# Kernel optimization log

Measured on AMD Instinct MI355X. Metric: run time of the kernel, lower is better.

Reference implementation:

```python
import jax, jax.numpy as jnp
import numpy as np

HIDDEN = 2048
HEAD_DIM = 128
N_HEADS = 16
ROPE_THETA = 150000.0
EPS = 1e-5
SEQ = 2048


def setup_inputs() -> dict:
    key = jax.random.key(0)
    k0, k1, k2 = jax.random.split(key, 3)
    x = jax.random.normal(k0, (SEQ, HIDDEN), jnp.float32)
    norm_scale = jnp.ones((HIDDEN,), jnp.float32)
    qkv_w = jax.random.normal(k1, (3 * HIDDEN, HIDDEN), jnp.float32) * 0.02
    qkv_b = jnp.zeros((3 * HIDDEN,), jnp.float32)
    out_w = jax.random.normal(k2, (HIDDEN, HIDDEN), jnp.float32) * 0.02
    out_b = jnp.zeros((HIDDEN,), jnp.float32)
    return {"x": x, "norm_scale": norm_scale, "qkv_w": qkv_w, "qkv_b": qkv_b,
            "out_w": out_w, "out_b": out_b}


def _rmsnorm(x, scale, eps=EPS):
    t = x * jax.lax.rsqrt(jnp.mean(x * x, axis=-1, keepdims=True) + eps)
    return t * scale


def _apply_rotary(x, cos, sin):
    # x: (n, H, d); cos/sin: (n, 1, d//2)  -- NeoX half-split rotary
    x1, x2 = jnp.split(x, 2, axis=-1)
    return jnp.concatenate([x1 * cos - x2 * sin, x2 * cos + x1 * sin], axis=-1)


def reference(x, norm_scale, qkv_w, qkv_b, out_w, out_b):
    n = x.shape[0]
    t = _rmsnorm(x, norm_scale)
    qkv = t @ qkv_w.T + qkv_b                      # (n, 3*hidden)
    q, k, v = jnp.split(qkv, 3, axis=-1)           # each (n, hidden)
    q = q.reshape(n, N_HEADS, HEAD_DIM)
    k = k.reshape(n, N_HEADS, HEAD_DIM)
    v = v.reshape(n, N_HEADS, HEAD_DIM)

    pos = jnp.arange(n, dtype=jnp.float32)
    inv = 1.0 / (ROPE_THETA ** (jnp.arange(0, HEAD_DIM, 2, dtype=jnp.float32) / HEAD_DIM))
    freqs = pos[:, None] * inv[None, :]            # (n, d//2)
    cos = jnp.cos(freqs)[:, None, :]
    sin = jnp.sin(freqs)[:, None, :]
    q = _apply_rotary(q, cos, sin)
    k = _apply_rotary(k, cos, sin)

    scale = 1.0 / np.sqrt(HEAD_DIM)
    att = jnp.einsum('qhd,khd->hqk', q, k) * scale  # (H, n, n) -- full score tensor as in source
    causal = jnp.tril(jnp.ones((n, n), dtype=bool))
    att = jnp.where(causal[None, :, :], att, -jnp.inf)
    w = jax.nn.softmax(att, axis=-1)
    o = jnp.einsum('hqk,khd->qhd', w, v).reshape(n, HIDDEN)
    return x + o @ out_w.T + out_b
```

## Files before the change

### kernel.cpp

```cpp
#include <hip/hip_runtime.h>
#include <math.h>

#define HIDDEN 2048
#define NHEADS 16
#define HD     128
#define QKV3   6144
#define EPSV   1e-5f
#define NEGBIG -30000.0f

typedef short bf16x8 __attribute__((ext_vector_type(8)));
typedef float f32x4  __attribute__((ext_vector_type(4)));

__device__ inline unsigned short f2bf(float f) {
    unsigned u = __float_as_uint(f);
    u += 0x7fff + ((u >> 16) & 1);
    return (unsigned short)(u >> 16);
}
__device__ inline float bf2f(unsigned short h) {
    return __uint_as_float(((unsigned)h) << 16);
}

union FragCast { uint4 u; bf16x8 v; };
__device__ inline bf16x8 as_frag(uint4 x) { FragCast c; c.u = x; return c.v; }
union U16x8 { unsigned short h[8]; uint4 v; };

__device__ __forceinline__ void gload16(const void* gsrc, void* ldst) {
    typedef __attribute__((address_space(1))) const char GC;
    typedef __attribute__((address_space(3))) char LC;
    __builtin_amdgcn_global_load_lds((GC*)(unsigned long long)gsrc,
                                     (LC*)(unsigned long long)ldst, 16, 0, 0);
}

__global__ __launch_bounds__(256) void f32_to_bf16_kernel(
        const float* __restrict__ in, unsigned short* __restrict__ out, int count) {
    int i = (blockIdx.x * 256 + threadIdx.x) * 4;
    if (i >= count) return;
    float4 v = *(const float4*)&in[i];
    ushort4 o = {f2bf(v.x), f2bf(v.y), f2bf(v.z), f2bf(v.w)};
    *(ushort4*)&out[i] = o;
}

__global__ void rope_table_kernel(float* __restrict__ cost, float* __restrict__ sint) {
    int pos = blockIdx.x;
    int i   = threadIdx.x;
    float inv = exp2f((float)i * (-17.1946030f / 64.0f));
    float f   = (float)pos * inv;
    cost[pos * 64 + i] = cosf(f);
    sint[pos * 64 + i] = sinf(f);
}

__global__ __launch_bounds__(256) void rmsnorm_kernel(
        const float* __restrict__ x, const float* __restrict__ scale,
        unsigned short* __restrict__ t) {
    int row = blockIdx.x;
    int tid = threadIdx.x;
    const float* xr = x + (size_t)row * HIDDEN;
    unsigned short* tr = t + (size_t)row * HIDDEN;

    float4 v[2];
    float ss = 0.f;
#pragma unroll
    for (int u = 0; u < 2; ++u) {
        v[u] = ((const float4*)xr)[tid + u * 256];
        ss += v[u].x * v[u].x + v[u].y * v[u].y + v[u].z * v[u].z + v[u].w * v[u].w;
    }
#pragma unroll
    for (int off = 32; off; off >>= 1) ss += __shfl_xor(ss, off);
    __shared__ float wsum[4];
    if ((tid & 63) == 0) wsum[tid >> 6] = ss;
    __syncthreads();
    float tot = wsum[0] + wsum[1] + wsum[2] + wsum[3];
    float r = rsqrtf(tot / (float)HIDDEN + EPSV);
#pragma unroll
    for (int u = 0; u < 2; ++u) {
        int idx = tid + u * 256;
        float4 sc = ((const float4*)scale)[idx];
        ushort4 o = {f2bf(v[u].x * r * sc.x), f2bf(v[u].y * r * sc.y),
                     f2bf(v[u].z * r * sc.z), f2bf(v[u].w * r * sc.w)};
        ((ushort4*)tr)[idx] = o;
    }
}

__global__ __launch_bounds__(256) void gemm_bf16_kernel(
        const unsigned short* __restrict__ A, const unsigned short* __restrict__ B,
        const float* __restrict__ bias, const float* __restrict__ resid,
        float* __restrict__ C, int M, int N, int K) {
    __shared__ __align__(16) unsigned short As[128][32];
    __shared__ __align__(16) unsigned short Bs[128][32];

    int tid  = threadIdx.x;
    int bn   = blockIdx.x * 128;
    int bm   = blockIdx.y * 128;
    int lane = tid & 63;
    int wid  = tid >> 6;
    int wr   = wid >> 1;
    int wc   = wid & 1;
    int fr   = lane & 15;
    int fq   = lane >> 4;

    f32x4 acc[4][4] = {};

    const int nk = K >> 5;
    for (int kt = 0; kt < nk; ++kt) {
        int k0 = kt << 5;
#pragma unroll
        for (int u = 0; u < 2; ++u) {
            int c   = tid + u * 256;
            int row = c >> 2;
            int kk  = (c & 3) * 8;
            gload16(&A[(size_t)(bm + row) * K + k0 + kk], &As[(wid << 4) + (u << 6)][0]);
            gload16(&B[(size_t)(bn + row) * K + k0 + kk], &Bs[(wid << 4) + (u << 6)][0]);
        }
        __syncthreads();

        bf16x8 af[4], bfr[4];
#pragma unroll
        for (int i = 0; i < 4; ++i) {
            af[i]  = as_frag(*(const uint4*)&As[wr * 64 + i * 16 + fr][fq * 8]);
            bfr[i] = as_frag(*(const uint4*)&Bs[wc * 64 + i * 16 + fr][fq * 8]);
        }
#pragma unroll
        for (int mi = 0; mi < 4; ++mi)
#pragma unroll
            for (int ni = 0; ni < 4; ++ni)
                acc[mi][ni] = __builtin_amdgcn_mfma_f32_16x16x32_bf16(
                    af[mi], bfr[ni], acc[mi][ni], 0, 0, 0);
        __syncthreads();
    }

#pragma unroll
    for (int ni = 0; ni < 4; ++ni) {
        int col = bn + wc * 64 + ni * 16 + fr;
        float bb = bias[col];
#pragma unroll
        for (int mi = 0; mi < 4; ++mi) {
#pragma unroll
            for (int r = 0; r < 4; ++r) {
                int row = bm + wr * 64 + mi * 16 + fq * 4 + r;
                float v = acc[mi][ni][r] + bb;
                if (resid) v += resid[(size_t)row * N + col];
                C[(size_t)row * N + col] = v;
            }
        }
    }
}

__global__ void repack_qk_kernel(const float* __restrict__ qkv,
                                 const float* __restrict__ cost,
                                 const float* __restrict__ sint,
                                 unsigned short* __restrict__ qb,
                                 unsigned short* __restrict__ kb, int n) {
    int pos = blockIdx.x, h = blockIdx.y;
    int t = threadIdx.x;
    int qk = t >> 6, i = t & 63;
    const float* src = qkv + (size_t)pos * QKV3 + qk * HIDDEN + h * HD;
    float c = cost[pos * 64 + i], s = sint[pos * 64 + i];
    float x1 = src[i], x2 = src[i + 64];
    float y1 = x1 * c - x2 * s, y2 = x2 * c + x1 * s;
    float sc = qk ? 1.0f : 0.088388347648318447f;
    unsigned short* dst = (qk ? kb : qb) + ((size_t)h * n + pos) * HD;
    dst[i]      = f2bf(y1 * sc);
    dst[i + 64] = f2bf(y2 * sc);
}

__global__ __launch_bounds__(256) void v_transpose_kernel(
        const float* __restrict__ qkv, unsigned short* __restrict__ vt, int n) {
    int n0 = blockIdx.x * 64;
    int d0 = blockIdx.y * 64;
    int h  = blockIdx.z;
    __shared__ float tile[64][68];
    int tid = threadIdx.x;
#pragma unroll
    for (int u = 0; u < 4; ++u) {
        int c = tid + u * 256;
        int r = c >> 4, c4 = (c & 15) * 4;
        *(float4*)&tile[r][c4] =
            *(const float4*)&qkv[(size_t)(n0 + r) * QKV3 + 2 * HIDDEN + h * HD + d0 + c4];
    }
    __syncthreads();
#pragma unroll
    for (int u = 0; u < 2; ++u) {
        int c = tid + u * 256;
        int d = c >> 3, nn = (c & 7) * 8;
        U16x8 o;
#pragma unroll
        for (int e = 0; e < 8; ++e) o.h[e] = f2bf(tile[nn + e][d]);
        *(uint4*)&vt[((size_t)h * HD + d0 + d) * n + n0 + nn] = o.v;
    }
}

#define QB  128
#define KVB 64
#define NSPLIT 4
__global__ __launch_bounds__(512) void attn_part_kernel(
        const unsigned short* __restrict__ qb_,
        const unsigned short* __restrict__ kb,
        const unsigned short* __restrict__ vt,
        unsigned short* __restrict__ o_part,
        float* __restrict__ m_part,
        float* __restrict__ l_part, int n) {
    int nqb  = n / QB;
    int fid  = blockIdx.x;
    int h    = fid & 15;
    int rest = fid >> 4;
    int qbi  = (nqb - 1) - (rest % nqb);
    int s    = rest / nqb;
    int q0   = qbi * QB;
    int ntiles = (q0 + QB) / KVB;
    int chunk  = (ntiles + NSPLIT - 1) >> 2;
    int t0 = s * chunk;
    int t1 = t0 + chunk; if (t1 > ntiles) t1 = ntiles;
    int tid = threadIdx.x;

    if (t0 >= ntiles) {
        if (tid < QB) {
            size_t idx = ((size_t)s * NHEADS + h) * n + q0 + tid;
            m_part[idx] = NEGBIG;
            l_part[idx] = 0.f;
            for (int e = 0; e < HD / 8; ++e) {
                U16x8 z; z.v = make_uint4(0, 0, 0, 0);
                *(uint4*)&o_part[idx * HD + e * 8] = z.v;
            }
        }
        return;
    }

    int lane = tid & 63, w = tid >> 6;
    int g = lane >> 4, i = lane & 15;
    int myrow0 = q0 + w * 16;

    __shared__ __align__(16) unsigned short Kb[KVB][136];
    __shared__ __align__(16) unsigned short Vt[128][72];
    __shared__ __align__(16) unsigned short Pl[8][16][72];

    bf16x8 qf[4];
    {
        const unsigned short* qrow = qb_ + ((size_t)h * n + myrow0 + i) * HD;
#pragma unroll
        for (int kk = 0; kk < 4; ++kk)
            qf[kk] = as_frag(*(const uint4*)&qrow[kk * 32 + 8 * g]);
    }

    f32x4 o_acc[8] = {};
    float m_r[4], l_r[4];
#pragma unroll
    for (int r = 0; r < 4; ++r) { m_r[r] = 0.f; l_r[r] = 0.f; }

    for (int kt = t0; kt < t1; ++kt) {
        int k0 = kt * KVB;
#pragma unroll
        for (int u = 0; u < 2; ++u) {
            int c = tid + u * 512;
            int row = c >> 4, col = (c & 15) * 8;
            *(uint4*)&Kb[row][col] =
                *(const uint4*)&kb[((size_t)h * n + k0 + row) * HD + col];
        }
#pragma unroll
        for (int u = 0; u < 2; ++u) {
            int c = tid + u * 512;
            int row = c >> 3, col = (c & 7) * 8;
            *(uint4*)&Vt[row][col] =
                *(const uint4*)&vt[((size_t)h * HD + row) * n + k0 + col];
        }
        __syncthreads();

        f32x4 s_acc[4] = {};
#pragma unroll
        for (int nb = 0; nb < 4; ++nb)
#pragma unroll
            for (int kk = 0; kk < 4; ++kk) {
                bf16x8 kf = as_frag(*(const uint4*)&Kb[nb * 16 + i][kk * 32 + 8 * g]);
                s_acc[nb] = __builtin_amdgcn_mfma_f32_16x16x32_bf16(
                    qf[kk], kf, s_acc[nb], 0, 0, 0);
            }

        bool diagzone = (kt >= ntiles - 2);
        float mx[4];
#pragma unroll
        for (int r = 0; r < 4; ++r) mx[r] = NEGBIG;
#pragma unroll
        for (int nb = 0; nb < 4; ++nb)
#pragma unroll
            for (int r = 0; r < 4; ++r) {
                float sv = s_acc[nb][r];
                if (diagzone && (k0 + nb * 16 + i > myrow0 + 4 * g + r)) sv = NEGBIG;
                s_acc[nb][r] = sv;
                mx[r] = fmaxf(mx[r], sv);
            }
#pragma unroll
        for (int off = 1; off < 16; off <<= 1)
#pragma unroll
            for (int r = 0; r < 4; ++r)
                mx[r] = fmaxf(mx[r], __shfl_xor(mx[r], off));

        float alpha[4], sum[4];
#pragma unroll
        for (int r = 0; r < 4; ++r) {
            float mnew = fmaxf(m_r[r], mx[r]);
            alpha[r] = __expf(m_r[r] - mnew);
            m_r[r] = mnew;
            sum[r] = 0.f;
        }
#pragma unroll
        for (int nb = 0; nb < 4; ++nb)
#pragma unroll
            for (int r = 0; r < 4; ++r) {
                float p = __expf(s_acc[nb][r] - m_r[r]);
                s_acc[nb][r] = p;
                sum[r] += p;
            }
#pragma unroll
        for (int off = 1; off < 16; off <<= 1)
#pragma unroll
            for (int r = 0; r < 4; ++r)
                sum[r] += __shfl_xor(sum[r], off);
#pragma unroll
        for (int r = 0; r < 4; ++r) l_r[r] = l_r[r] * alpha[r] + sum[r];

#pragma unroll
        for (int d0 = 0; d0 < 8; ++d0)
#pragma unroll
            for (int r = 0; r < 4; ++r)
                o_acc[d0][r] *= alpha[r];

#pragma unroll
        for (int nb = 0; nb < 4; ++nb)
#pragma unroll
            for (int r = 0; r < 4; ++r)
                Pl[w][4 * g + r][nb * 16 + i] = f2bf(s_acc[nb][r]);
        __builtin_amdgcn_sched_barrier(0);

#pragma unroll
        for (int kk = 0; kk < 2; ++kk) {
            bf16x8 pf = as_frag(*(const uint4*)&Pl[w][i][kk * 32 + 8 * g]);
#pragma unroll
            for (int d0 = 0; d0 < 8; ++d0) {
                bf16x8 vf = as_frag(*(const uint4*)&Vt[d0 * 16 + i][kk * 32 + 8 * g]);
                o_acc[d0] = __builtin_amdgcn_mfma_f32_16x16x32_bf16(
                    pf, vf, o_acc[d0], 0, 0, 0);
            }
        }
        __syncthreads();
    }

#pragma unroll
    for (int r = 0; r < 4; ++r) {
        int q = myrow0 + 4 * g + r;
        size_t idx = ((size_t)s * NHEADS + h) * n + q;
#pragma unroll
        for (int d0 = 0; d0 < 8; ++d0)
            o_part[idx * HD + d0 * 16 + i] = f2bf(o_acc[d0][r]);
        if (i == 0) { m_part[idx] = m_r[r]; l_part[idx] = l_r[r]; }
    }
}

__global__ __launch_bounds__(256) void attn_combine_kernel(
        const unsigned short* __restrict__ o_part,
        const float* __restrict__ m_part, const float* __restrict__ l_part,
        unsigned short* __restrict__ ob, int n) {
    int q = blockIdx.x;
    int t = threadIdx.x;
    int h = t >> 4;
    int d = (t & 15) * 8;

    float m[NSPLIT], mstar = NEGBIG;
#pragma unroll
    for (int s = 0; s < NSPLIT; ++s) {
        m[s] = m_part[((size_t)s * NHEADS + h) * n + q];
        mstar = fmaxf(mstar, m[s]);
    }
    float l = 0.f, o[8] = {};
#pragma unroll
    for (int s = 0; s < NSPLIT; ++s) {
        if (m[s] < -1e4f) continue;
        float ws = __expf(m[s] - mstar);
        l += ws * l_part[((size_t)s * NHEADS + h) * n + q];
        U16x8 ov;
        ov.v = *(const uint4*)&o_part[(((size_t)s * NHEADS + h) * n + q) * HD + d];
#pragma unroll
        for (int e = 0; e < 8; ++e) o[e] += ws * bf2f(ov.h[e]);
    }
    float inv = 1.f / l;
    U16x8 w8;
#pragma unroll
    for (int e = 0; e < 8; ++e) w8.h[e] = f2bf(o[e] * inv);
    *(uint4*)&ob[(size_t)q * HIDDEN + h * HD + d] = w8.v;
}

extern "C" void kernel_launch(void* const* d_in, const int* in_sizes, int n_in,
                              void* d_out, int out_size, void* d_ws, size_t ws_size,
                              hipStream_t stream) {
    const float* x     = (const float*)d_in[0];
    const float* nsc   = (const float*)d_in[1];
    const float* qkv_w = (const float*)d_in[2];
    const float* qkv_b = (const float*)d_in[3];
    const float* out_w = (const float*)d_in[4];
    const float* out_b = (const float*)d_in[5];
    float* out = (float*)d_out;
    int n = in_sizes[0] / HIDDEN;

    char* w = (char*)d_ws;
    float* qkv  = (float*)w;  w += (size_t)n * QKV3 * 4;
    float* cost = (float*)w;  w += (size_t)n * 64 * 4;
    float* sint = (float*)w;  w += (size_t)n * 64 * 4;
    unsigned short* wq = (unsigned short*)w;
    unsigned short* qb = wq;
    unsigned short* kb = qb + (size_t)n * HIDDEN;
    unsigned short* vt = kb + (size_t)n * HIDDEN;
    size_t unionBytes = (size_t)QKV3 * HIDDEN * 2;
    size_t need3      = (size_t)3 * n * HIDDEN * 2;
    w += (unionBytes > need3 ? unionBytes : need3);
    unsigned short* wo = (unsigned short*)w;  w += (size_t)HIDDEN * HIDDEN * 2;
    unsigned short* tb = (unsigned short*)w;
    unsigned short* ob = tb;

    unsigned short* o_part = (unsigned short*)qkv;
    float* m_part = (float*)((char*)qkv + (size_t)NSPLIT * NHEADS * n * HD * 2);
    float* l_part = m_part + (size_t)NSPLIT * NHEADS * n;

    f32_to_bf16_kernel<<<(QKV3 * HIDDEN) / 1024, 256, 0, stream>>>(qkv_w, wq, QKV3 * HIDDEN);
    f32_to_bf16_kernel<<<(HIDDEN * HIDDEN) / 1024, 256, 0, stream>>>(out_w, wo, HIDDEN * HIDDEN);
    rope_table_kernel<<<n, 64, 0, stream>>>(cost, sint);
    rmsnorm_kernel<<<n, 256, 0, stream>>>(x, nsc, tb);
    gemm_bf16_kernel<<<dim3(QKV3 / 128, n / 128), 256, 0, stream>>>(
        tb, wq, qkv_b, nullptr, qkv, n, QKV3, HIDDEN);
    repack_qk_kernel<<<dim3(n, NHEADS), 128, 0, stream>>>(qkv, cost, sint, qb, kb, n);
    v_transpose_kernel<<<dim3(n / 64, HD / 64, NHEADS), 256, 0, stream>>>(qkv, vt, n);
    attn_part_kernel<<<dim3((n / QB) * NHEADS * NSPLIT), 512, 0, stream>>>(
        qb, kb, vt, o_part, m_part, l_part, n);
    attn_combine_kernel<<<n, 256, 0, stream>>>(o_part, m_part, l_part, ob, n);
    gemm_bf16_kernel<<<dim3(HIDDEN / 128, n / 128), 256, 0, stream>>>(
        ob, wo, out_b, x, out, n, HIDDEN, HIDDEN);
}
```

Before: 270.3 us.

## Double-buffer GEMM LDS tiles with async prefetch two stages ahead

Converts the bf16 GEMM's single shared-memory tile into a two-slot ring. Global-to-LDS loads for tile kt+2 are issued while MFMAs run on the current tile, with explicit vmcnt waits and barriers replacing __syncthreads. The goal is to hide global load latency behind compute. It doubles LDS use per block, which may lower occupancy, and it relies on hand-counted vmcnt values being correct for gload16.

```diff
diff --git a/kernel.cpp b/kernel.cpp
--- a/kernel.cpp
+++ b/kernel.cpp
@@ -85,8 +85,8 @@
         const unsigned short* __restrict__ A, const unsigned short* __restrict__ B,
         const float* __restrict__ bias, const float* __restrict__ resid,
         float* __restrict__ C, int M, int N, int K) {
-    __shared__ __align__(16) unsigned short As[128][32];
-    __shared__ __align__(16) unsigned short Bs[128][32];
+    __shared__ __align__(16) unsigned short As[2][128][32];
+    __shared__ __align__(16) unsigned short Bs[2][128][32];
 
     int tid  = threadIdx.x;
     int bn   = blockIdx.x * 128;
@@ -98,26 +98,35 @@
     int fr   = lane & 15;
     int fq   = lane >> 4;
 
-    f32x4 acc[4][4] = {};
-
-    const int nk = K >> 5;
-    for (int kt = 0; kt < nk; ++kt) {
+    auto stage = [&](int b, int kt) {
         int k0 = kt << 5;
 #pragma unroll
         for (int u = 0; u < 2; ++u) {
             int c   = tid + u * 256;
             int row = c >> 2;
             int kk  = (c & 3) * 8;
-            gload16(&A[(size_t)(bm + row) * K + k0 + kk], &As[(wid << 4) + (u << 6)][0]);
-            gload16(&B[(size_t)(bn + row) * K + k0 + kk], &Bs[(wid << 4) + (u << 6)][0]);
-        }
-        __syncthreads();
-
+            gload16(&A[(size_t)(bm + row) * K + k0 + kk], &As[b][(wid << 4) + (u << 6)][0]);
+            gload16(&B[(size_t)(bn + row) * K + k0 + kk], &Bs[b][(wid << 4) + (u << 6)][0]);
+        }
+    };
+
+    f32x4 acc[4][4] = {};
+    const int nk = K >> 5;
+
+    stage(0, 0);
+    stage(1, 1);
+    asm volatile("s_waitcnt vmcnt(4)" ::: "memory");
+    __builtin_amdgcn_sched_barrier(0);
+    __builtin_amdgcn_s_barrier();
+    __builtin_amdgcn_sched_barrier(0);
+
+    for (int kt = 0; kt < nk; ++kt) {
+        int cur = kt & 1;
         bf16x8 af[4], bfr[4];
 #pragma unroll
         for (int i = 0; i < 4; ++i) {
-            af[i]  = as_frag(*(const uint4*)&As[wr * 64 + i * 16 + fr][fq * 8]);
-            bfr[i] = as_frag(*(const uint4*)&Bs[wc * 64 + i * 16 + fr][fq * 8]);
+            af[i]  = as_frag(*(const uint4*)&As[cur][wr * 64 + i * 16 + fr][fq * 8]);
+            bfr[i] = as_frag(*(const uint4*)&Bs[cur][wc * 64 + i * 16 + fr][fq * 8]);
         }
 #pragma unroll
         for (int mi = 0; mi < 4; ++mi)
@@ -125,7 +134,19 @@
             for (int ni = 0; ni < 4; ++ni)
                 acc[mi][ni] = __builtin_amdgcn_mfma_f32_16x16x32_bf16(
                     af[mi], bfr[ni], acc[mi][ni], 0, 0, 0);
-        __syncthreads();
+        asm volatile("s_waitcnt lgkmcnt(0)" ::: "memory");
+        __builtin_amdgcn_sched_barrier(0);
+        __builtin_amdgcn_s_barrier();
+        __builtin_amdgcn_sched_barrier(0);
+        if (kt + 2 < nk) {
+            stage(cur, kt + 2);
+            asm volatile("s_waitcnt vmcnt(4)" ::: "memory");
+        } else {
+            asm volatile("s_waitcnt vmcnt(0)" ::: "memory");
+        }
+        __builtin_amdgcn_sched_barrier(0);
+        __builtin_amdgcn_s_barrier();
+        __builtin_amdgcn_sched_barrier(0);
     }
 
 #pragma unroll
```

After: 277.0 us. 2.5% more time.

## Fuse RoPE, Q scaling and V transpose into the QKV GEMM epilogue

Applied to the files above, without the earlier changes.

The QKV GEMM now writes its output as bf16 into an LDS tile. From there each block applies rotary embedding and the Q scale and writes to qb/kb, or transposes V into vt. This removes the fp32 qkv intermediate, which is roughly 50MB of global writes plus re-reads, and drops two separate kernel launches. The workspace is re-laid out so o_part reuses the bf16 weight and norm buffers and m/l reuse the rope tables. Q and K are now rounded to bf16 before rotary is applied, adding one extra rounding step.

```diff
diff --git a/kernel.cpp b/kernel.cpp
--- a/kernel.cpp
+++ b/kernel.cpp
@@ -145,47 +145,111 @@
     }
 }
 
-__global__ void repack_qk_kernel(const float* __restrict__ qkv,
-                                 const float* __restrict__ cost,
-                                 const float* __restrict__ sint,
-                                 unsigned short* __restrict__ qb,
-                                 unsigned short* __restrict__ kb, int n) {
-    int pos = blockIdx.x, h = blockIdx.y;
-    int t = threadIdx.x;
-    int qk = t >> 6, i = t & 63;
-    const float* src = qkv + (size_t)pos * QKV3 + qk * HIDDEN + h * HD;
-    float c = cost[pos * 64 + i], s = sint[pos * 64 + i];
-    float x1 = src[i], x2 = src[i + 64];
-    float y1 = x1 * c - x2 * s, y2 = x2 * c + x1 * s;
-    float sc = qk ? 1.0f : 0.088388347648318447f;
-    unsigned short* dst = (qk ? kb : qb) + ((size_t)h * n + pos) * HD;
-    dst[i]      = f2bf(y1 * sc);
-    dst[i + 64] = f2bf(y2 * sc);
-}
-
-__global__ __launch_bounds__(256) void v_transpose_kernel(
-        const float* __restrict__ qkv, unsigned short* __restrict__ vt, int n) {
-    int n0 = blockIdx.x * 64;
-    int d0 = blockIdx.y * 64;
-    int h  = blockIdx.z;
-    __shared__ float tile[64][68];
-    int tid = threadIdx.x;
-#pragma unroll
-    for (int u = 0; u < 4; ++u) {
-        int c = tid + u * 256;
-        int r = c >> 4, c4 = (c & 15) * 4;
-        *(float4*)&tile[r][c4] =
-            *(const float4*)&qkv[(size_t)(n0 + r) * QKV3 + 2 * HIDDEN + h * HD + d0 + c4];
+__global__ __launch_bounds__(256) void gemm_qkv_fused_kernel(
+        const unsigned short* __restrict__ A,
+        const unsigned short* __restrict__ B,
+        const float* __restrict__ bias,
+        const float* __restrict__ cost, const float* __restrict__ sint,
+        unsigned short* __restrict__ qb, unsigned short* __restrict__ kb,
+        unsigned short* __restrict__ vt, int n) {
+    const int K = HIDDEN;
+    __shared__ __align__(16) char smem[33792];
+    auto As = (unsigned short(*)[32])smem;
+    auto Bs = (unsigned short(*)[32])(smem + 8192);
+    auto Ct = (unsigned short(*)[132])smem;
+
+    int tid  = threadIdx.x;
+    int bn   = blockIdx.x * 128;
+    int bm   = blockIdx.y * 128;
+    int lane = tid & 63;
+    int wid  = tid >> 6;
+    int wr   = wid >> 1;
+    int wc   = wid & 1;
+    int fr   = lane & 15;
+    int fq   = lane >> 4;
+
+    f32x4 acc[4][4] = {};
+
+    const int nk = K >> 5;
+    for (int kt = 0; kt < nk; ++kt) {
+        int k0 = kt << 5;
+#pragma unroll
+        for (int u = 0; u < 2; ++u) {
+            int c   = tid + u * 256;
+            int row = c >> 2;
+            int kk  = (c & 3) * 8;
+            gload16(&A[(size_t)(bm + row) * K + k0 + kk], &As[(wid << 4) + (u << 6)][0]);
+            gload16(&B[(size_t)(bn + row) * K + k0 + kk], &Bs[(wid << 4) + (u << 6)][0]);
+        }
+        __syncthreads();
+
+        bf16x8 af[4], bfr[4];
+#pragma unroll
+        for (int i = 0; i < 4; ++i) {
+            af[i]  = as_frag(*(const uint4*)&As[wr * 64 + i * 16 + fr][fq * 8]);
+            bfr[i] = as_frag(*(const uint4*)&Bs[wc * 64 + i * 16 + fr][fq * 8]);
+        }
+#pragma unroll
+        for (int mi = 0; mi < 4; ++mi)
+#pragma unroll
+            for (int ni = 0; ni < 4; ++ni)
+                acc[mi][ni] = __builtin_amdgcn_mfma_f32_16x16x32_bf16(
+                    af[mi], bfr[ni], acc[mi][ni], 0, 0, 0);
+        __syncthreads();
+    }
+
+#pragma unroll
+    for (int ni = 0; ni < 4; ++ni) {
+        int lc = wc * 64 + ni * 16 + fr;
+        float bb = bias[bn + lc];
+#pragma unroll
+        for (int mi = 0; mi < 4; ++mi)
+#pragma unroll
+            for (int r = 0; r < 4; ++r)
+                Ct[wr * 64 + mi * 16 + fq * 4 + r][lc] = f2bf(acc[mi][ni][r] + bb);
     }
     __syncthreads();
-#pragma unroll
-    for (int u = 0; u < 2; ++u) {
-        int c = tid + u * 256;
-        int d = c >> 3, nn = (c & 7) * 8;
-        U16x8 o;
-#pragma unroll
-        for (int e = 0; e < 8; ++e) o.h[e] = f2bf(tile[nn + e][d]);
-        *(uint4*)&vt[((size_t)h * HD + d0 + d) * n + n0 + nn] = o.v;
+
+    int region = bn >> 11;
+    int h      = (bn & 2047) >> 7;
+    if (region == 2) {
+#pragma unroll
+        for (int u = 0; u < 8; ++u) {
+            int c2 = tid + u * 256;
+            int d  = c2 >> 4;
+            int r0 = (c2 & 15) * 8;
+            U16x8 o;
+#pragma unroll
+            for (int e = 0; e < 8; ++e) o.h[e] = Ct[r0 + e][d];
+            *(uint4*)&vt[((size_t)h * HD + d) * n + bm + r0] = o.v;
+        }
+    } else {
+        unsigned short* dst = region ? kb : qb;
+        float scq = region ? 1.0f : 0.088388347648318447f;
+#pragma unroll
+        for (int u = 0; u < 4; ++u) {
+            int t2 = tid + u * 256;
+            int rr = t2 >> 3;
+            int d0 = (t2 & 7) * 8;
+            int pos = bm + rr;
+            float4 c0 = *(const float4*)&cost[pos * 64 + d0];
+            float4 c1 = *(const float4*)&cost[pos * 64 + d0 + 4];
+            float4 s0 = *(const float4*)&sint[pos * 64 + d0];
+            float4 s1 = *(const float4*)&sint[pos * 64 + d0 + 4];
+            float cv[8] = {c0.x, c0.y, c0.z, c0.w, c1.x, c1.y, c1.z, c1.w};
+            float sv[8] = {s0.x, s0.y, s0.z, s0.w, s1.x, s1.y, s1.z, s1.w};
+            U16x8 lo, hi;
+#pragma unroll
+            for (int e = 0; e < 8; ++e) {
+                float x1 = bf2f(Ct[rr][d0 + e]);
+                float x2 = bf2f(Ct[rr][d0 + 64 + e]);
+                lo.h[e] = f2bf((x1 * cv[e] - x2 * sv[e]) * scq);
+                hi.h[e] = f2bf((x2 * cv[e] + x1 * sv[e]) * scq);
+            }
+            unsigned short* drow = dst + ((size_t)h * n + pos) * HD;
+            *(uint4*)&drow[d0]      = lo.v;
+            *(uint4*)&drow[d0 + 64] = hi.v;
+        }
     }
 }
 
@@ -400,32 +464,26 @@
     int n = in_sizes[0] / HIDDEN;
 
     char* w = (char*)d_ws;
-    float* qkv  = (float*)w;  w += (size_t)n * QKV3 * 4;
-    float* cost = (float*)w;  w += (size_t)n * 64 * 4;
-    float* sint = (float*)w;  w += (size_t)n * 64 * 4;
-    unsigned short* wq = (unsigned short*)w;
-    unsigned short* qb = wq;
-    unsigned short* kb = qb + (size_t)n * HIDDEN;
-    unsigned short* vt = kb + (size_t)n * HIDDEN;
-    size_t unionBytes = (size_t)QKV3 * HIDDEN * 2;
-    size_t need3      = (size_t)3 * n * HIDDEN * 2;
-    w += (unionBytes > need3 ? unionBytes : need3);
+    unsigned short* wq = (unsigned short*)w;  w += (size_t)QKV3 * HIDDEN * 2;
+    unsigned short* tb = (unsigned short*)w;  w += (size_t)2048 * HIDDEN * 2;
     unsigned short* wo = (unsigned short*)w;  w += (size_t)HIDDEN * HIDDEN * 2;
-    unsigned short* tb = (unsigned short*)w;
-    unsigned short* ob = tb;
-
-    unsigned short* o_part = (unsigned short*)qkv;
-    float* m_part = (float*)((char*)qkv + (size_t)NSPLIT * NHEADS * n * HD * 2);
-    float* l_part = m_part + (size_t)NSPLIT * NHEADS * n;
+    unsigned short* qb = (unsigned short*)w;  w += (size_t)n * HIDDEN * 2;
+    unsigned short* kb = (unsigned short*)w;  w += (size_t)n * HIDDEN * 2;
+    unsigned short* vt = (unsigned short*)w;  w += (size_t)n * HIDDEN * 2;
+    float* cost = (float*)w;                  w += (size_t)n * 64 * 4;
+    float* sint = (float*)w;                  w += (size_t)n * 64 * 4;
+    unsigned short* ob = (unsigned short*)w;  w += (size_t)n * HIDDEN * 2;
+
+    unsigned short* o_part = wq;
+    float* m_part = cost;
+    float* l_part = sint;
 
     f32_to_bf16_kernel<<<(QKV3 * HIDDEN) / 1024, 256, 0, stream>>>(qkv_w, wq, QKV3 * HIDDEN);
     f32_to_bf16_kernel<<<(HIDDEN * HIDDEN) / 1024, 256, 0, stream>>>(out_w, wo, HIDDEN * HIDDEN);
     rope_table_kernel<<<n, 64, 0, stream>>>(cost, sint);
     rmsnorm_kernel<<<n, 256, 0, stream>>>(x, nsc, tb);
-    gemm_bf16_kernel<<<dim3(QKV3 / 128, n / 128), 256, 0, stream>>>(
-        tb, wq, qkv_b, nullptr, qkv, n, QKV3, HIDDEN);
-    repack_qk_kernel<<<dim3(n, NHEADS), 128, 0, stream>>>(qkv, cost, sint, qb, kb, n);
-    v_transpose_kernel<<<dim3(n / 64, HD / 64, NHEADS), 256, 0, stream>>>(qkv, vt, n);
+    gemm_qkv_fused_kernel<<<dim3(QKV3 / 128, n / 128), 256, 0, stream>>>(
+        tb, wq, qkv_b, cost, sint, qb, kb, vt, n);
     attn_part_kernel<<<dim3((n / QB) * NHEADS * NSPLIT), 512, 0, stream>>>(
         qb, kb, vt, o_part, m_part, l_part, n);
     attn_combine_kernel<<<n, 256, 0, stream>>>(o_part, m_part, l_part, ob, n);
```

Result: faster. 227.4 us (-15.9%).
